# Performance work log

Measured on AMD Instinct MI355X. Metric: run time of the kernel, lower is better.

## Reference

```python
import jax, jax.numpy as jnp
import numpy as np

DIM = 1024
N_HEADS = 16
HEAD_DIM = DIM // N_HEADS
MLP_RATIO = 4
LN_EPS = 1e-5


def _layer_norm(x, w):
    xf = x.astype(jnp.float32)
    mu = jnp.mean(xf, axis=-1, keepdims=True)
    var = jnp.var(xf, axis=-1, keepdims=True)
    y = (xf - mu) / jnp.sqrt(var + LN_EPS)
    return y * w[None, None, :]


def _apply_rope(x, cos, sin):
    # x: (b, s, h, d); cos, sin: (s, d/2)
    c = jnp.concatenate([cos, cos], axis=-1)[None, :, None, :]  # (1,s,1,d)
    s_ = jnp.concatenate([sin, sin], axis=-1)[None, :, None, :]
    x1, x2 = jnp.split(x, 2, axis=-1)
    rot = jnp.concatenate([-x2, x1], axis=-1)
    return x * c + rot * s_


def setup_inputs() -> dict:
    key = jax.random.key(0)
    ks = jax.random.split(key, 12)
    b, s = 2, 2048
    x = jax.random.normal(ks[0], (b, s, DIM), dtype=jnp.float32)
    rot_cos = jax.random.uniform(ks[1], (1, s, 1, 1, HEAD_DIM), dtype=jnp.float32)
    rot_sin = jax.random.uniform(ks[2], (1, s, 1, 1, HEAD_DIM), dtype=jnp.float32)
    w_init = 0.02
    params = {
        'ln1_w': jnp.ones((DIM,), jnp.float32),
        'w_qkv': jax.random.normal(ks[3], (3 * DIM, DIM), jnp.float32) * w_init,
        'w_out': jax.random.normal(ks[4], (DIM, DIM), jnp.float32) * w_init,
        'ln2_w': jnp.ones((DIM,), jnp.float32),
        'w_mlp1': jax.random.normal(ks[5], (MLP_RATIO * DIM, DIM), jnp.float32) * w_init,
        'b_mlp1': jnp.zeros((MLP_RATIO * DIM,), jnp.float32),
        'w_mlp2': jax.random.normal(ks[6], (DIM, MLP_RATIO * DIM), jnp.float32) * w_init,
        'b_mlp2': jnp.zeros((DIM,), jnp.float32),
    }
    return {'x': x, 'rot_cos': rot_cos, 'rot_sin': rot_sin, **params}


def reference(x, rot_cos, rot_sin, ln1_w, w_qkv, w_out, ln2_w, w_mlp1, b_mlp1, w_mlp2, b_mlp2):
    b, s, _ = x.shape
    # _split_rotary: (1,s,1,1,hd) -> (s, hd/2)
    cos = rot_cos[0, :, 0, 0, : HEAD_DIM // 2]
    sin = rot_sin[0, :, 0, 0, : HEAD_DIM // 2]

    x_skip = x
    h1 = _layer_norm(x, ln1_w)
    qkv = jnp.einsum('bsd,ed->bse', h1, w_qkv).reshape(b, s, 3, N_HEADS, HEAD_DIM)
    q, k, v = qkv[:, :, 0], qkv[:, :, 1], qkv[:, :, 2]
    q = _apply_rope(q, cos, sin)
    k = _apply_rope(k, cos, sin)

    # causal SDPA, scale = 1/sqrt(head_dim) (flex_attention default)
    scale = 1.0 / np.sqrt(HEAD_DIM)
    scores = jnp.einsum('bqhd,bkhd->bhqk', q, k) * scale
    causal = jnp.tril(jnp.ones((s, s), dtype=bool))
    scores = jnp.where(causal[None, None], scores, -jnp.inf)
    attn = jax.nn.softmax(scores, axis=-1)
    o = jnp.einsum('bhqk,bkhd->bqhd', attn, v).reshape(b, s, DIM)

    # attn out + residual (eval: dropout off, scale=1)
    x = x_skip + jnp.einsum('bsd,ed->bse', o, w_out)

    # MLP with tanh GELU + residual
    h2 = _layer_norm(x, ln2_w)
    u = jnp.einsum('bsd,ed->bse', h2, w_mlp1) + b_mlp1
    u = jax.nn.gelu(u, approximate=True)
    m = jnp.einsum('bse,de->bsd', u, w_mlp2) + b_mlp2
    return x + m
```

## Files before the change

### kernel.cpp

```cpp
#include <hip/hip_runtime.h>
#include <hip/hip_bf16.h>
#include <math.h>


#define B_ 2
#define S_ 2048
#define D_ 1024
#define H_ 16
#define DH_ 64
#define MLP_ 4096
#define ROWS_ (B_ * S_)

typedef short bf16x8 __attribute__((ext_vector_type(8)));
typedef float f32x4 __attribute__((ext_vector_type(4)));
typedef unsigned short ushort_t;
typedef ushort_t u16x4 __attribute__((ext_vector_type(4)));
typedef unsigned int u32x2 __attribute__((ext_vector_type(2)));

__device__ __forceinline__ float wave_reduce_sum(float v) {
  #pragma unroll
  for (int off = 32; off > 0; off >>= 1) v += __shfl_down(v, off, 64);
  return v;
}

__device__ __forceinline__ ushort_t f2bf(float v) {
  __hip_bfloat16 h = __float2bfloat16(v);
  return *(ushort_t*)&h;
}
__device__ __forceinline__ float bf2f(ushort_t u) {
  unsigned int v = ((unsigned int)u) << 16;
  union { unsigned int i; float f; } c; c.i = v; return c.f;
}

__device__ __forceinline__ float exp2_fast(float x) {
#if __has_builtin(__builtin_amdgcn_exp2f)
  return __builtin_amdgcn_exp2f(x);
#else
  return exp2f(x);
#endif
}
__device__ __forceinline__ float rcp_fast(float x) {
#if __has_builtin(__builtin_amdgcn_rcpf)
  return __builtin_amdgcn_rcpf(x);
#else
  return 1.0f / x;
#endif
}

__device__ __forceinline__ void async_copy16(const void* g, void* l) {
  __builtin_amdgcn_global_load_lds(
      (const __attribute__((address_space(1))) void*)g,
      (__attribute__((address_space(3))) void*)l, 16, 0, 0);
}

__global__ __launch_bounds__(256) void cast_w_kernel(
    const float* __restrict__ s0, ushort_t* __restrict__ d0, int n0,
    const float* __restrict__ s1, ushort_t* __restrict__ d1, int n1,
    const float* __restrict__ s2, ushort_t* __restrict__ d2, int n2,
    const float* __restrict__ s3, ushort_t* __restrict__ d3, int n3) {
  const float* s; ushort_t* d; int n;
  switch (blockIdx.y) {
    case 0: s = s0; d = d0; n = n0; break;
    case 1: s = s1; d = d1; n = n1; break;
    case 2: s = s2; d = d2; n = n2; break;
    default: s = s3; d = d3; n = n3; break;
  }
  const int i = (blockIdx.x * 256 + threadIdx.x) * 4;
  if (i < n) {
    const float4 v = *reinterpret_cast<const float4*>(s + i);
    u16x4 o;
    o[0] = f2bf(v.x); o[1] = f2bf(v.y); o[2] = f2bf(v.z); o[3] = f2bf(v.w);
    *reinterpret_cast<u16x4*>(d + i) = o;
  }
}

__global__ __launch_bounds__(256) void ln_kernel(
    const float* __restrict__ x, const float* __restrict__ w,
    ushort_t* __restrict__ y) {
  const int row = blockIdx.x;
  const float4 v = reinterpret_cast<const float4*>(x + (size_t)row * D_)[threadIdx.x];
  float s  = v.x + v.y + v.z + v.w;
  float ss = v.x * v.x + v.y * v.y + v.z * v.z + v.w * v.w;
  __shared__ float red[8];
  const int wave = threadIdx.x >> 6, lane = threadIdx.x & 63;
  const float ws1 = wave_reduce_sum(s);
  const float ws2 = wave_reduce_sum(ss);
  if (lane == 0) { red[wave] = ws1; red[4 + wave] = ws2; }
  __syncthreads();
  const float tot  = red[0] + red[1] + red[2] + red[3];
  const float tot2 = red[4] + red[5] + red[6] + red[7];
  const float mu  = tot * (1.0f / D_);
  const float var = tot2 * (1.0f / D_) - mu * mu;
  const float inv = rsqrtf(var + 1e-5f);
  const float4 wv = reinterpret_cast<const float4*>(w)[threadIdx.x];
  u16x4 o;
  o[0] = f2bf((v.x - mu) * inv * wv.x);
  o[1] = f2bf((v.y - mu) * inv * wv.y);
  o[2] = f2bf((v.z - mu) * inv * wv.z);
  o[3] = f2bf((v.w - mu) * inv * wv.w);
  reinterpret_cast<u16x4*>(y + (size_t)row * D_)[threadIdx.x] = o;
}

__device__ __forceinline__ float gelu_tanh(float u) {
  const float p = u + 0.044715f * u * u * u;
  const float e = exp2_fast(-2.3022078f * p);
  return u * rcp_fast(1.0f + e);
}

template <int FUSE, int OUTBF, int QKV>
__global__ __launch_bounds__(256) void gemm_bt(
    const ushort_t* __restrict__ A, const ushort_t* __restrict__ W,
    const float* __restrict__ bias, const float* __restrict__ res,
    void* __restrict__ Cv, ushort_t* __restrict__ VtOut,
    const float* __restrict__ cosb, const float* __restrict__ sinb,
    ushort_t* __restrict__ Qo, ushort_t* __restrict__ Ko,
    int M, int N, int K, int sm, int sn, int rects_n) {
  __shared__ ushort_t As[3][128 * 32];
  __shared__ ushort_t Bs[3][128 * 32];
  const int tid = threadIdx.x;
  const int wave = tid >> 6, lane = tid & 63;
  const int l15 = lane & 15, quad = lane >> 4;

  const int lin = blockIdx.x;
  const int xcd = lin & 7, j = lin >> 3;
  const int rm = xcd / rects_n, rn = xcd % rects_n;
  const int m0 = (rm * sm + (j % sm)) * 128;
  const int n0 = (rn * sn + (j / sm)) * 128;
  const int wm = (wave & 1) * 64, wn = (wave >> 1) * 64;

  const int srow = tid >> 2;
  const int gcol = (((tid & 3) ^ ((srow >> 1) & 3)) * 8);
  const ushort_t* Ag = A + (size_t)(m0 + srow) * K + gcol;
  const ushort_t* Wg = W + (size_t)(n0 + srow) * K + gcol;

  f32x4 acc[4][4] = {};
  const int rslot = (quad ^ ((l15 >> 1) & 3)) * 8;

  const int NI = K >> 5;
  async_copy16(Ag,               &As[0][tid * 8]);
  async_copy16(Ag + 64 * K,      &As[0][2048 + tid * 8]);
  async_copy16(Wg,               &Bs[0][tid * 8]);
  async_copy16(Wg + 64 * K,      &Bs[0][2048 + tid * 8]);
  if (NI > 1) {
    async_copy16(Ag + 32,          &As[1][tid * 8]);
    async_copy16(Ag + 64 * K + 32, &As[1][2048 + tid * 8]);
    async_copy16(Wg + 32,          &Bs[1][tid * 8]);
    async_copy16(Wg + 64 * K + 32, &Bs[1][2048 + tid * 8]);
  }

  int st = 0;
  for (int i = 0; i < NI; ++i) {
    if (i + 1 < NI) asm volatile("s_waitcnt vmcnt(4)" ::: "memory");
    else            asm volatile("s_waitcnt vmcnt(0)" ::: "memory");
    __builtin_amdgcn_s_barrier();
    __builtin_amdgcn_sched_barrier(0);
    if (i + 2 < NI) {
      const int k2 = (i + 2) << 5;
      const int nb = (st >= 1) ? st - 1 : st + 2;
      async_copy16(Ag + k2,          &As[nb][tid * 8]);
      async_copy16(Ag + 64 * K + k2, &As[nb][2048 + tid * 8]);
      async_copy16(Wg + k2,          &Bs[nb][tid * 8]);
      async_copy16(Wg + 64 * K + k2, &Bs[nb][2048 + tid * 8]);
    }
    bf16x8 af[4], bfr[4];
    #pragma unroll
    for (int ii = 0; ii < 4; ++ii) {
      af[ii]  = *(const bf16x8*)&As[st][(wm + ii * 16 + l15) * 32 + rslot];
      bfr[ii] = *(const bf16x8*)&Bs[st][(wn + ii * 16 + l15) * 32 + rslot];
    }
    #pragma unroll
    for (int ii = 0; ii < 4; ++ii)
      #pragma unroll
      for (int jj = 0; jj < 4; ++jj)
        acc[ii][jj] = __builtin_amdgcn_mfma_f32_16x16x32_bf16(af[ii], bfr[jj], acc[ii][jj], 0, 0, 0);
    st = (st == 2) ? 0 : st + 1;
  }

  const int nsec = QKV ? ((n0 + wn) >> 10) : 0;

  #pragma unroll
  for (int i = 0; i < 4; ++i) {
    const int mb = m0 + wm + i * 16 + quad * 4;
    if (QKV && nsec != 2) {
      const int hh = ((n0 + wn) >> 6) & 15;
      const int bb = mb >> 11;
      const int s0r = mb & (S_ - 1);
      ushort_t* dst = (nsec == 0) ? Qo : Ko;
      const float qs = (nsec == 0) ? 0.18033688736f : 1.0f;
      #pragma unroll
      for (int r = 0; r < 4; ++r) {
        const int s = s0r + r;
        const float c0 = cosb[s * 64 + l15];
        const float c1 = cosb[s * 64 + 16 + l15];
        const float sn0 = sinb[s * 64 + l15];
        const float sn1 = sinb[s * 64 + 16 + l15];
        const float v0 = acc[i][0][r], v1 = acc[i][1][r];
        const float v2 = acc[i][2][r], v3 = acc[i][3][r];
        const size_t base = (((size_t)(bb * H_ + hh) * S_ + s)) * DH_ + l15;
        dst[base]      = f2bf((v0 * c0 - v2 * sn0) * qs);
        dst[base + 16] = f2bf((v1 * c1 - v3 * sn1) * qs);
        dst[base + 32] = f2bf((v2 * c0 + v0 * sn0) * qs);
        dst[base + 48] = f2bf((v3 * c1 + v1 * sn1) * qs);
      }
      continue;
    }
    #pragma unroll
    for (int jj = 0; jj < 4; ++jj) {
      const int n = n0 + wn + jj * 16 + l15;
      float cv[4];
      #pragma unroll
      for (int r = 0; r < 4; ++r) {
        float c = acc[i][jj][r];
        if (FUSE & 1) c += bias[n];
        if (FUSE & 2) c = gelu_tanh(c);
        if (FUSE & 4) c += res[(size_t)(mb + r) * N + n];
        cv[r] = c;
      }
      if (QKV && nsec == 2) {
        const int d  = n & 63;
        const int hh = (n >> 6) & 15;
        const int bb = mb >> 11;
        const int ss = mb & (S_ - 1);
        u16x4 pk;
        #pragma unroll
        for (int r = 0; r < 4; ++r) pk[r] = f2bf(cv[r]);
        *(u16x4*)&VtOut[((size_t)(bb * H_ + hh) * DH_ + d) * S_ + ss] = pk;
      } else {
        #pragma unroll
        for (int r = 0; r < 4; ++r) {
          if (OUTBF) ((ushort_t*)Cv)[(size_t)(mb + r) * N + n] = f2bf(cv[r]);
          else       ((float*)Cv)[(size_t)(mb + r) * N + n]   = cv[r];
        }
      }
    }
  }
}

template <int FUSE, int OUTBF>
__global__ __launch_bounds__(512) void gemm64_bt(
    const ushort_t* __restrict__ A, const ushort_t* __restrict__ W,
    const float* __restrict__ bias, const float* __restrict__ res,
    void* __restrict__ Cv, int M, int N, int K, int sm, int sn, int rects_n) {
  __shared__ ushort_t As[3][64 * 64];
  __shared__ ushort_t Bs[3][128 * 64];
  const int tid = threadIdx.x;
  const int wave = tid >> 6, lane = tid & 63;
  const int l15 = lane & 15, quad = lane >> 4;

  const int lin = blockIdx.x;
  const int xcd = lin & 7, j = lin >> 3;
  const int rm = xcd / rects_n, rn = xcd % rects_n;
  const int m0 = (rm * sm + (j % sm)) * 64;
  const int n0 = (rn * sn + (j / sm)) * 128;
  const int wm = (wave & 1) * 32;
  const int wn = (wave >> 1) * 32;

  const int srow = tid >> 3;
  const int scol = (((tid & 7) ^ (srow & 7)) * 8);
  const ushort_t* Ag = A + (size_t)(m0 + srow) * K + scol;
  const ushort_t* Wg = W + (size_t)(n0 + srow) * K + scol;

  f32x4 acc[2][2] = {};

  const int NI = K >> 6;
  async_copy16(Ag,           &As[0][tid * 8]);
  async_copy16(Wg,           &Bs[0][tid * 8]);
  async_copy16(Wg + 64 * K,  &Bs[0][4096 + tid * 8]);
  if (NI > 1) {
    async_copy16(Ag + 64,          &As[1][tid * 8]);
    async_copy16(Wg + 64,          &Bs[1][tid * 8]);
    async_copy16(Wg + 64 * K + 64, &Bs[1][4096 + tid * 8]);
  }

  int st = 0;
  for (int it = 0; it < NI; ++it) {
    if (it + 1 < NI) asm volatile("s_waitcnt vmcnt(3)" ::: "memory");
    else             asm volatile("s_waitcnt vmcnt(0)" ::: "memory");
    __builtin_amdgcn_s_barrier();
    __builtin_amdgcn_sched_barrier(0);
    if (it + 2 < NI) {
      const int k2 = (it + 2) << 6;
      const int nb = (st >= 1) ? st - 1 : st + 2;
      async_copy16(Ag + k2,          &As[nb][tid * 8]);
      async_copy16(Wg + k2,          &Bs[nb][tid * 8]);
      async_copy16(Wg + 64 * K + k2, &Bs[nb][4096 + tid * 8]);
    }
    #pragma unroll
    for (int kk = 0; kk < 2; ++kk) {
      const int slot = (((kk * 4 + quad) ^ (l15 & 7)) * 8);
      bf16x8 af[2], bfr[2];
      #pragma unroll
      for (int i = 0; i < 2; ++i)
        af[i] = *(const bf16x8*)&As[st][(wm + i * 16 + l15) * 64 + slot];
      #pragma unroll
      for (int jj = 0; jj < 2; ++jj)
        bfr[jj] = *(const bf16x8*)&Bs[st][(wn + jj * 16 + l15) * 64 + slot];
      #pragma unroll
      for (int i = 0; i < 2; ++i)
        #pragma unroll
        for (int jj = 0; jj < 2; ++jj)
          acc[i][jj] = __builtin_amdgcn_mfma_f32_16x16x32_bf16(af[i], bfr[jj], acc[i][jj], 0, 0, 0);
    }
    st = (st == 2) ? 0 : st + 1;
  }

  #pragma unroll
  for (int i = 0; i < 2; ++i) {
    const int mb = m0 + wm + i * 16 + quad * 4;
    #pragma unroll
    for (int jj = 0; jj < 2; ++jj) {
      const int n = n0 + wn + jj * 16 + l15;
      #pragma unroll
      for (int r = 0; r < 4; ++r) {
        float c = acc[i][jj][r];
        if (FUSE & 1) c += bias[n];
        if (FUSE & 2) c = gelu_tanh(c);
        if (FUSE & 4) c += res[(size_t)(mb + r) * N + n];
        if (OUTBF) ((ushort_t*)Cv)[(size_t)(mb + r) * N + n] = f2bf(c);
        else       ((float*)Cv)[(size_t)(mb + r) * N + n]   = c;
      }
    }
  }
}

#define PPAD 72

__global__ __launch_bounds__(512) void attn_kernel(
    const ushort_t* __restrict__ Qb, const ushort_t* __restrict__ Kb,
    const ushort_t* __restrict__ Vt, ushort_t* __restrict__ O) {
  __shared__ ushort_t Ks[2][64 * 64];
  __shared__ ushort_t Vs[2][64 * 64];
  __shared__ ushort_t Plds[8][16 * PPAD];

  const int tid  = threadIdx.x;
  const int wave = tid >> 6;
  const int lane = tid & 63;
  const int l15 = lane & 15, quad = lane >> 4;

  const int lin = blockIdx.x;
  const int bh  = lin & 31;
  const int u   = lin >> 5;
  const int g   = (u < 8) ? (15 - u) : (u - 8);
  const int b = bh >> 4, h = bh & 15;
  const int q0 = g * 128 + wave * 16;

  const int nch_w   = (q0 >> 6) + 1;
  const int nch_max = 2 * g + 2;

  const ushort_t* Kbh = Kb + (size_t)bh * S_ * DH_;
  const ushort_t* Vbh = Vt + (size_t)bh * DH_ * S_;

  auto stage = [&](int buf, int c) {
    const int k0s = c << 6;
    const int row  = tid >> 3;
    const int slot = tid & 7;
    const int scol = ((slot ^ (row & 7)) * 8);
    async_copy16(Kbh + (size_t)(k0s + row) * DH_ + scol, &Ks[buf][tid * 8]);
    async_copy16(Vbh + (size_t)row * S_ + k0s + scol,    &Vs[buf][tid * 8]);
  };

  bf16x8 qb[2];
  {
    const ushort_t* qptr = Qb + ((size_t)bh * S_ + q0 + l15) * DH_ + quad * 8;
    qb[0] = *(const bf16x8*)(qptr);
    qb[1] = *(const bf16x8*)(qptr + 32);
  }

  f32x4 o_acc[4] = {};
  float m_run = -1e30f, l_run = 0.0f;

  stage(0, 0);

  for (int c = 0; c < nch_max; ++c) {
    const int st = c & 1;
    __syncthreads();
    if (c + 1 < nch_max) stage(st ^ 1, c + 1);
    if (c >= nch_w) continue;
    const int k0 = c << 6;

    bf16x8 ka[4][2];
    #pragma unroll
    for (int kt = 0; kt < 4; ++kt) {
      const int row = kt * 16 + l15;
      const int bse = row * 64, rx = row & 7;
      ka[kt][0] = *(const bf16x8*)&Ks[st][bse + ((quad ^ rx) * 8)];
      ka[kt][1] = *(const bf16x8*)&Ks[st][bse + (((4 + quad) ^ rx) * 8)];
    }

    f32x4 s_t[4];
    __builtin_amdgcn_s_setprio(1);
    #pragma unroll
    for (int kt = 0; kt < 4; ++kt) {
      f32x4 z = {0.0f, 0.0f, 0.0f, 0.0f};
      z = __builtin_amdgcn_mfma_f32_16x16x32_bf16(ka[kt][0], qb[0], z, 0, 0, 0);
      z = __builtin_amdgcn_mfma_f32_16x16x32_bf16(ka[kt][1], qb[1], z, 0, 0, 0);
      s_t[kt] = z;
    }
    __builtin_amdgcn_s_setprio(0);

    if (c == nch_w - 1) {
      const int query = q0 + l15;
      #pragma unroll
      for (int kt = 0; kt < 4; ++kt)
        #pragma unroll
        for (int r = 0; r < 4; ++r)
          if (k0 + kt * 16 + quad * 4 + r > query) s_t[kt][r] = -1e30f;
    }

    {
      float mx = -1e30f;
      #pragma unroll
      for (int kt = 0; kt < 4; ++kt)
        #pragma unroll
        for (int r = 0; r < 4; ++r) mx = fmaxf(mx, s_t[kt][r]);
      mx = fmaxf(mx, __shfl_xor(mx, 16, 64));
      mx = fmaxf(mx, __shfl_xor(mx, 32, 64));
      if (!__all(mx <= m_run + 8.0f)) {
        const float m_new = fmaxf(m_run, mx);
        const float alpha = exp2_fast(m_run - m_new);
        l_run *= alpha;
        #pragma unroll
        for (int mt = 0; mt < 4; ++mt)
          #pragma unroll
          for (int r = 0; r < 4; ++r) o_acc[mt][r] *= alpha;
        m_run = m_new;
      }
      float rs = 0.0f;
      #pragma unroll
      for (int kt = 0; kt < 4; ++kt)
        #pragma unroll
        for (int r = 0; r < 4; ++r) {
          const float e = exp2_fast(s_t[kt][r] - m_run);
          s_t[kt][r] = e;
          rs += e;
        }
      rs += __shfl_xor(rs, 16, 64);
      rs += __shfl_xor(rs, 32, 64);
      l_run += rs;
    }

    bf16x8 va[4][2];
    #pragma unroll
    for (int mt = 0; mt < 4; ++mt) {
      const int row = mt * 16 + l15;
      const int bse = row * 64, rx = row & 7;
      va[mt][0] = *(const bf16x8*)&Vs[st][bse + ((quad ^ rx) * 8)];
      va[mt][1] = *(const bf16x8*)&Vs[st][bse + (((4 + quad) ^ rx) * 8)];
    }

    {
      ushort_t* Pw = &Plds[wave][0];
      #pragma unroll
      for (int kt = 0; kt < 4; ++kt) {
        u32x2 wpair;
        wpair[0] = (unsigned)f2bf(s_t[kt][0]) | ((unsigned)f2bf(s_t[kt][1]) << 16);
        wpair[1] = (unsigned)f2bf(s_t[kt][2]) | ((unsigned)f2bf(s_t[kt][3]) << 16);
        *(u32x2*)&Pw[l15 * PPAD + kt * 16 + quad * 4] = wpair;
      }
      asm volatile("s_waitcnt lgkmcnt(0)" ::: "memory");
      const bf16x8 pb0 = *(const bf16x8*)&Pw[l15 * PPAD + quad * 8];
      const bf16x8 pb1 = *(const bf16x8*)&Pw[l15 * PPAD + 32 + quad * 8];
      __builtin_amdgcn_s_setprio(1);
      #pragma unroll
      for (int mt = 0; mt < 4; ++mt) {
        o_acc[mt] = __builtin_amdgcn_mfma_f32_16x16x32_bf16(va[mt][0], pb0, o_acc[mt], 0, 0, 0);
        o_acc[mt] = __builtin_amdgcn_mfma_f32_16x16x32_bf16(va[mt][1], pb1, o_acc[mt], 0, 0, 0);
      }
      __builtin_amdgcn_s_setprio(0);
    }
  }

  {
    const float inv = 1.0f / l_run;
    #pragma unroll
    for (int mt = 0; mt < 4; ++mt) {
      u16x4 pk;
      #pragma unroll
      for (int r = 0; r < 4; ++r) pk[r] = f2bf(o_acc[mt][r] * inv);
      *(u16x4*)&O[(((size_t)b * S_ + q0 + l15) * H_ + h) * DH_ + mt * 16 + quad * 4] = pk;
    }
  }
}

extern "C" void kernel_launch(void* const* d_in, const int* in_sizes, int n_in,
                              void* d_out, int out_size, void* d_ws, size_t ws_size,
                              hipStream_t stream) {
  const float* x       = (const float*)d_in[0];
  const float* rot_cos = (const float*)d_in[1];
  const float* rot_sin = (const float*)d_in[2];
  const float* ln1_w   = (const float*)d_in[3];
  const float* w_qkv   = (const float*)d_in[4];
  const float* w_out   = (const float*)d_in[5];
  const float* ln2_w   = (const float*)d_in[6];
  const float* w_mlp1  = (const float*)d_in[7];
  const float* b_mlp1  = (const float*)d_in[8];
  const float* w_mlp2  = (const float*)d_in[9];
  const float* b_mlp2  = (const float*)d_in[10];
  float* out = (float*)d_out;

  char* wsb = (char*)d_ws;
  const size_t MB = 1u << 20;
  ushort_t* h1_bf  = (ushort_t*)(wsb + 0 * MB);
  ushort_t* q_bf   = (ushort_t*)(wsb + 32 * MB);
  ushort_t* k_bf   = (ushort_t*)(wsb + 40 * MB);
  ushort_t* v_t    = (ushort_t*)(wsb + 48 * MB);
  ushort_t* o_bf   = (ushort_t*)(wsb + 56 * MB);
  float*    x2     = (float*)   (wsb + 64 * MB);
  ushort_t* u_bf   = (ushort_t*)(wsb + 80 * MB);
  ushort_t* wq_bf  = (ushort_t*)(wsb + 112 * MB);
  ushort_t* wo_bf  = (ushort_t*)(wsb + 118 * MB);
  ushort_t* w1_bf  = (ushort_t*)(wsb + 120 * MB);
  ushort_t* w2_bf  = (ushort_t*)(wsb + 128 * MB);
  (void)ws_size; (void)in_sizes; (void)n_in; (void)out_size;

  dim3 b256(256);

  cast_w_kernel<<<dim3(4096, 4), b256, 0, stream>>>(
      w_qkv, wq_bf, 3 * D_ * D_, w_out, wo_bf, D_ * D_,
      w_mlp1, w1_bf, MLP_ * D_, w_mlp2, w2_bf, MLP_ * D_);
  ln_kernel<<<dim3(ROWS_), b256, 0, stream>>>(x, ln1_w, h1_bf);
  gemm_bt<0, 1, 1><<<dim3(768), b256, 0, stream>>>(
      h1_bf, wq_bf, nullptr, nullptr, nullptr, v_t,
      rot_cos, rot_sin, q_bf, k_bf, ROWS_, 3 * D_, D_, 16, 6, 4);
  attn_kernel<<<dim3(512), dim3(512), 0, stream>>>(q_bf, k_bf, v_t, o_bf);
  gemm64_bt<4, 0><<<dim3(512), dim3(512), 0, stream>>>(
      o_bf, wo_bf, nullptr, x, x2, ROWS_, D_, D_, 16, 4, 2);
  ln_kernel<<<dim3(ROWS_), b256, 0, stream>>>(x2, ln2_w, h1_bf);
  gemm_bt<3, 1, 0><<<dim3(1024), b256, 0, stream>>>(
      h1_bf, w1_bf, b_mlp1, nullptr, u_bf, nullptr,
      nullptr, nullptr, nullptr, nullptr, ROWS_, MLP_, D_, 16, 8, 4);
  gemm64_bt<5, 0><<<dim3(512), dim3(512), 0, stream>>>(
      u_bf, w2_bf, b_mlp2, x2, out, ROWS_, D_, MLP_, 16, 4, 2);
}
```

Baseline: 331.0 us.

## Load A operand directly from global into registers in gemm64_bt, drop LDS staging

The 64x128 GEMM kernel stops staging the A tile through shared memory. Each wave now loads its own A fragments straight from global memory into registers, double-buffered one iteration ahead, and only B goes through the async LDS ring. Launch bounds now request 4 blocks per SM. This removes A's LDS writes and reads and frees shared memory for occupancy, at the cost of uncoalesced 16-byte global loads, A rows read redundantly by waves sharing them, and hand-tuned vmcnt waits that assume NI is even.

```diff
diff --git a/kernel.cpp b/kernel.cpp
--- a/kernel.cpp
+++ b/kernel.cpp
@@ -237,11 +237,10 @@
 }
 
 template <int FUSE, int OUTBF>
-__global__ __launch_bounds__(512) void gemm64_bt(
+__global__ __launch_bounds__(512, 4) void gemm64_bt(
     const ushort_t* __restrict__ A, const ushort_t* __restrict__ W,
     const float* __restrict__ bias, const float* __restrict__ res,
     void* __restrict__ Cv, int M, int N, int K, int sm, int sn, int rects_n) {
-  __shared__ ushort_t As[3][64 * 64];
   __shared__ ushort_t Bs[3][128 * 64];
   const int tid = threadIdx.x;
   const int wave = tid >> 6, lane = tid & 63;
@@ -257,41 +256,51 @@
 
   const int srow = tid >> 3;
   const int scol = (((tid & 7) ^ (srow & 7)) * 8);
-  const ushort_t* Ag = A + (size_t)(m0 + srow) * K + scol;
   const ushort_t* Wg = W + (size_t)(n0 + srow) * K + scol;
 
+  const ushort_t* Aw = A + (size_t)(m0 + wm + l15) * K + quad * 8;
+
   f32x4 acc[2][2] = {};
-
   const int NI = K >> 6;
-  async_copy16(Ag,           &As[0][tid * 8]);
-  async_copy16(Wg,           &Bs[0][tid * 8]);
-  async_copy16(Wg + 64 * K,  &Bs[0][4096 + tid * 8]);
-  if (NI > 1) {
-    async_copy16(Ag + 64,          &As[1][tid * 8]);
-    async_copy16(Wg + 64,          &Bs[1][tid * 8]);
-    async_copy16(Wg + 64 * K + 64, &Bs[1][4096 + tid * 8]);
-  }
-
-  int st = 0;
-  for (int it = 0; it < NI; ++it) {
-    if (it + 1 < NI) asm volatile("s_waitcnt vmcnt(3)" ::: "memory");
-    else             asm volatile("s_waitcnt vmcnt(0)" ::: "memory");
+
+  bf16x8 aP[2][2], aQ[2][2];
+
+  auto loadA = [&](bf16x8 (&dst)[2][2], int it) {
+    const int k0 = it << 6;
+    #pragma unroll
+    for (int i = 0; i < 2; ++i)
+      #pragma unroll
+      for (int kk = 0; kk < 2; ++kk)
+        dst[i][kk] = *(const bf16x8*)(Aw + (size_t)(i * 16) * K + k0 + kk * 32);
+  };
+  auto stageB = [&](int buf, int it) {
+    const int k0 = it << 6;
+    async_copy16(Wg + k0,          &Bs[buf][tid * 8]);
+    async_copy16(Wg + 64 * K + k0, &Bs[buf][4096 + tid * 8]);
+  };
+
+  loadA(aP, 0);
+  __builtin_amdgcn_sched_barrier(0);
+  stageB(0, 0);
+  __builtin_amdgcn_sched_barrier(0);
+  stageB(1, 1);
+
+  auto body = [&](bf16x8 (&cur)[2][2], bf16x8 (&nxt)[2][2], int it, int st) {
+    if (it == 0)          asm volatile("s_waitcnt vmcnt(2)" ::: "memory");
+    else if (it + 1 < NI) asm volatile("s_waitcnt vmcnt(6)" ::: "memory");
+    else                  asm volatile("s_waitcnt vmcnt(4)" ::: "memory");
     __builtin_amdgcn_s_barrier();
     __builtin_amdgcn_sched_barrier(0);
+    if (it + 1 < NI) loadA(nxt, it + 1);
+    __builtin_amdgcn_sched_barrier(0);
     if (it + 2 < NI) {
-      const int k2 = (it + 2) << 6;
       const int nb = (st >= 1) ? st - 1 : st + 2;
-      async_copy16(Ag + k2,          &As[nb][tid * 8]);
-      async_copy16(Wg + k2,          &Bs[nb][tid * 8]);
-      async_copy16(Wg + 64 * K + k2, &Bs[nb][4096 + tid * 8]);
+      stageB(nb, it + 2);
     }
     #pragma unroll
     for (int kk = 0; kk < 2; ++kk) {
       const int slot = (((kk * 4 + quad) ^ (l15 & 7)) * 8);
-      bf16x8 af[2], bfr[2];
-      #pragma unroll
-      for (int i = 0; i < 2; ++i)
-        af[i] = *(const bf16x8*)&As[st][(wm + i * 16 + l15) * 64 + slot];
+      bf16x8 bfr[2];
       #pragma unroll
       for (int jj = 0; jj < 2; ++jj)
         bfr[jj] = *(const bf16x8*)&Bs[st][(wn + jj * 16 + l15) * 64 + slot];
@@ -299,9 +308,14 @@
       for (int i = 0; i < 2; ++i)
         #pragma unroll
         for (int jj = 0; jj < 2; ++jj)
-          acc[i][jj] = __builtin_amdgcn_mfma_f32_16x16x32_bf16(af[i], bfr[jj], acc[i][jj], 0, 0, 0);
-    }
-    st = (st == 2) ? 0 : st + 1;
+          acc[i][jj] = __builtin_amdgcn_mfma_f32_16x16x32_bf16(cur[i][kk], bfr[jj], acc[i][jj], 0, 0, 0);
+    }
+  };
+
+  int st = 0;
+  for (int it = 0; it < NI; it += 2) {
+    body(aP, aQ, it, st);     st = (st == 2) ? 0 : st + 1;
+    body(aQ, aP, it + 1, st); st = (st == 2) ? 0 : st + 1;
   }
 
   #pragma unroll
```

Result: slower. 440.7 us (+33.2%).
